# Kernel optimization log

Hardware: AMD Instinct MI355X
Metric: run time of the kernel (lower is better)

Reference implementation:

```python
import jax, jax.numpy as jnp
import numpy as np
import math

N_EMBD = 1024
N_HEAD = 16
B, T = 4, 2048

def setup_inputs() -> dict:
    key = jax.random.key(0)
    k1, k2, k3, k4 = jax.random.split(key, 4)
    x = jax.random.normal(k1, (B, T, N_EMBD), dtype=jnp.float32)
    # torch Linear weights: [out, in]; init scale ~1/sqrt(in)
    s = 1.0 / math.sqrt(N_EMBD)
    W_attn = jax.random.normal(k2, (3 * N_EMBD, N_EMBD), dtype=jnp.float32) * s
    W_proj = jax.random.normal(k3, (N_EMBD, N_EMBD), dtype=jnp.float32) * s
    b_proj = jax.random.normal(k4, (N_EMBD,), dtype=jnp.float32) * s
    return {"x": x, "W_attn": W_attn, "W_proj": W_proj, "b_proj": b_proj}

def reference(x, W_attn, W_proj, b_proj):
    Bx, Tx, C = x.shape
    hd = C // N_HEAD
    qkv = jnp.einsum('btc,oc->bto', x, W_attn)  # [B,T,3C]
    q, k, v = jnp.split(qkv, 3, axis=2)
    # [B, H, T, hd]
    q = q.reshape(Bx, Tx, N_HEAD, hd).transpose(0, 2, 1, 3)
    k = k.reshape(Bx, Tx, N_HEAD, hd).transpose(0, 2, 1, 3)
    v = v.reshape(Bx, Tx, N_HEAD, hd).transpose(0, 2, 1, 3)
    # NOTE: source divides by (1/sqrt(hd)) => MULTIPLIES by sqrt(hd). Faithful.
    att = jnp.einsum('bhqd,bhkd->bhqk', q, k) * jnp.sqrt(jnp.float32(hd))
    causal = jnp.tril(jnp.ones((Tx, Tx), dtype=bool))
    att = jnp.where(causal[None, None, :, :], att, -jnp.inf)
    att = jax.nn.softmax(att, axis=-1)
    y = jnp.einsum('bhqk,bhkd->bhqd', att, v)
    y = y.transpose(0, 2, 1, 3).reshape(Bx, Tx, C)
    y = jnp.einsum('btc,oc->bto', y, W_proj) + b_proj
    return y  # dropout is identity in eval
```

## Files before the change

kernel.cpp:

```cpp
#include <hip/hip_runtime.h>
#include <math.h>

#define BATCH 4
#define TSEQ  2048
#define CEMB  1024
#define NHEAD 16
#define HD    64
#define MROWS (BATCH * TSEQ)

typedef _Float16 half8 __attribute__((ext_vector_type(8)));
typedef _Float16 half4 __attribute__((ext_vector_type(4)));
typedef float    floatx4 __attribute__((ext_vector_type(4)));

#define GLOBAL_AS __attribute__((address_space(1)))
#define LDS_AS    __attribute__((address_space(3)))

__device__ __forceinline__ void lds_dma16(const _Float16* g, _Float16* l) {
    __builtin_amdgcn_global_load_lds((const GLOBAL_AS unsigned int*)g,
                                     (LDS_AS unsigned int*)l, 16, 0, 0);
}

__global__ __launch_bounds__(256)
void cvt_fp16(const float* __restrict__ x, const float* __restrict__ wa,
              const float* __restrict__ wp, _Float16* __restrict__ x16,
              _Float16* __restrict__ wa16, _Float16* __restrict__ wp16)
{
    const int n1 = (BATCH * TSEQ * CEMB) / 4;
    const int n2 = (3 * CEMB * CEMB) / 4;
    int i = blockIdx.x * 256 + threadIdx.x;
    const float* src; _Float16* dst; int j;
    if (i < n1)            { src = x;  dst = x16;  j = i; }
    else if (i < n1 + n2)  { src = wa; dst = wa16; j = i - n1; }
    else                   { src = wp; dst = wp16; j = i - n1 - n2; }
    float4 v = ((const float4*)src)[j];
    half4 h = { (_Float16)v.x, (_Float16)v.y, (_Float16)v.z, (_Float16)v.w };
    ((half4*)dst)[j] = h;
}

__device__ __forceinline__ void stage32(const _Float16* __restrict__ gbase,
                                        _Float16* __restrict__ lds,
                                        int row0, int kk, int tid)
{
#pragma unroll
    for (int p = 0; p < 2; ++p) {
        int ci  = p * 256 + tid;
        int row = ci >> 2, pcc = ci & 3;
        int c   = pcc ^ (row & 3);
        lds_dma16(gbase + (size_t)(row0 + row) * CEMB + kk + c * 8, lds + ci * 8);
    }
}

__device__ __forceinline__ void gemm_frags(const _Float16* __restrict__ As,
                                           const _Float16* __restrict__ Bs,
                                           int wm, int wn, int l15, int quad,
                                           half8 (&af)[4], half8 (&bf)[4])
{
#pragma unroll
    for (int mt = 0; mt < 4; ++mt) {
        int row = wm * 64 + mt * 16 + l15;
        af[mt] = *(const half8*)(As + row * 32 + (quad ^ (row & 3)) * 8);
    }
#pragma unroll
    for (int nt = 0; nt < 4; ++nt) {
        int row = wn * 64 + nt * 16 + l15;
        bf[nt] = *(const half8*)(Bs + row * 32 + (quad ^ (row & 3)) * 8);
    }
}

__global__ __launch_bounds__(256)
void qkv_gemm(const _Float16* __restrict__ A, const _Float16* __restrict__ B,
              _Float16* __restrict__ q16, _Float16* __restrict__ k16,
              _Float16* __restrict__ v16)
{
    __shared__ __align__(16) _Float16 As[2][128 * 32];
    __shared__ __align__(16) _Float16 Bs[2][128 * 32];
    const int tid = threadIdx.x, lane = tid & 63, wave = tid >> 6;
    const int wm = wave & 1, wn = wave >> 1;
    const int m0 = blockIdx.y * 128, n0 = blockIdx.x * 128;
    const int l15 = lane & 15, quad = lane >> 4;

    floatx4 acc[4][4];
#pragma unroll
    for (int i = 0; i < 4; ++i)
#pragma unroll
        for (int j = 0; j < 4; ++j) acc[i][j] = (floatx4){0.f, 0.f, 0.f, 0.f};

    stage32(A, As[0], m0, 0, tid);
    stage32(B, Bs[0], n0, 0, tid);
    for (int kt = 0; kt < 32; ++kt) {
        const int cur = kt & 1;
        __syncthreads();
        if (kt < 31) {
            stage32(A, As[cur ^ 1], m0, (kt + 1) * 32, tid);
            stage32(B, Bs[cur ^ 1], n0, (kt + 1) * 32, tid);
        }
        half8 af[4], bf[4];
        gemm_frags(As[cur], Bs[cur], wm, wn, l15, quad, af, bf);
#pragma unroll
        for (int mt = 0; mt < 4; ++mt)
#pragma unroll
            for (int nt = 0; nt < 4; ++nt)
                acc[mt][nt] = __builtin_amdgcn_mfma_f32_16x16x32_f16(af[mt], bf[nt], acc[mt][nt], 0, 0, 0);
    }

    const int rbase = quad << 2;
#pragma unroll
    for (int mt = 0; mt < 4; ++mt) {
#pragma unroll
        for (int nt = 0; nt < 4; ++nt) {
            int gn = n0 + wn * 64 + nt * 16 + l15;
#pragma unroll
            for (int r = 0; r < 4; ++r) {
                int gm = m0 + wm * 64 + mt * 16 + rbase + r;
                int b = gm >> 11, t = gm & (TSEQ - 1);
                if (gn < CEMB) {
                    int h = gn >> 6, d = gn & 63;
                    q16[(((size_t)(b * NHEAD + h)) * TSEQ + t) * HD + d] =
                        (_Float16)(acc[mt][nt][r] * 8.0f);
                } else if (gn < 2 * CEMB) {
                    int c2 = gn - CEMB;
                    int h = c2 >> 6, d = c2 & 63;
                    k16[(((size_t)(b * NHEAD + h)) * TSEQ + t) * HD + d] =
                        (_Float16)acc[mt][nt][r];
                } else {
                    int c2 = gn - 2 * CEMB;
                    int h = c2 >> 6, d = c2 & 63;
                    v16[(((size_t)(b * NHEAD + h)) * HD + d) * TSEQ + t] =
                        (_Float16)acc[mt][nt][r];
                }
            }
        }
    }
}

__device__ __forceinline__ void attn_tile(
    const half8& qf0, const half8& qf1,
    float& m_i, float& l_i, floatx4 (&o)[4],
    const _Float16* __restrict__ Ks, const _Float16* __restrict__ Vs,
    bool domask, int l15, int quad, int relq)
{
    floatx4 s[4];
#pragma unroll
    for (int nt = 0; nt < 4; ++nt) {
        int row = nt * 16 + l15;
        int pc0 = quad ^ (row & 7);
        half8 kf0 = *(const half8*)(Ks + row * 64 + pc0 * 8);
        half8 kf1 = *(const half8*)(Ks + row * 64 + (pc0 ^ 4) * 8);
        floatx4 z = (floatx4){0.f, 0.f, 0.f, 0.f};
        z = __builtin_amdgcn_mfma_f32_16x16x32_f16(kf0, qf0, z, 0, 0, 0);
        z = __builtin_amdgcn_mfma_f32_16x16x32_f16(kf1, qf1, z, 0, 0, 0);
        s[nt] = z;
    }
    if (domask) {
#pragma unroll
        for (int nt = 0; nt < 4; ++nt)
#pragma unroll
            for (int r = 0; r < 4; ++r)
                if (nt * 16 + quad * 4 + r > relq) s[nt][r] = -INFINITY;
    }
    float mx = m_i;
#pragma unroll
    for (int nt = 0; nt < 4; ++nt)
        mx = fmaxf(mx, fmaxf(fmaxf(s[nt][0], s[nt][1]), fmaxf(s[nt][2], s[nt][3])));
    mx = fmaxf(mx, __shfl_xor(mx, 16, 64));
    mx = fmaxf(mx, __shfl_xor(mx, 32, 64));
    float alpha = __expf(m_i - mx);
    m_i = mx;
    float rs = 0.f;
    half4 p[4];
#pragma unroll
    for (int nt = 0; nt < 4; ++nt) {
        float p0 = __expf(s[nt][0] - mx), p1 = __expf(s[nt][1] - mx);
        float p2 = __expf(s[nt][2] - mx), p3 = __expf(s[nt][3] - mx);
        rs += (p0 + p1) + (p2 + p3);
        p[nt] = (half4){ (_Float16)p0, (_Float16)p1, (_Float16)p2, (_Float16)p3 };
    }
    rs += __shfl_xor(rs, 16, 64);
    rs += __shfl_xor(rs, 32, 64);
    l_i = l_i * alpha + rs;
#pragma unroll
    for (int mt = 0; mt < 4; ++mt)
#pragma unroll
        for (int r = 0; r < 4; ++r) o[mt][r] *= alpha;
#pragma unroll
    for (int mt = 0; mt < 4; ++mt) {
        int d = mt * 16 + l15;
#pragma unroll
        for (int nt = 0; nt < 4; ++nt) {
            int pc = (2 * nt + (quad >> 1)) ^ (d & 7);
            half4 vf = *(const half4*)(Vs + d * 64 + pc * 8 + (quad & 1) * 4);
            o[mt] = __builtin_amdgcn_mfma_f32_16x16x16f16(vf, p[nt], o[mt], 0, 0, 0);
        }
    }
}

__global__ __launch_bounds__(256)
void attn_fwd(const _Float16* __restrict__ q16, const _Float16* __restrict__ k16,
              const _Float16* __restrict__ v16, _Float16* __restrict__ o16)
{
    __shared__ __align__(16) _Float16 Ks[2][64 * 64];
    __shared__ __align__(16) _Float16 Vs[2][64 * 64];
    const int tid = threadIdx.x, lane = tid & 63, wave = tid >> 6;
    const int l15 = lane & 15, quad = lane >> 4;
    const int qtA = blockIdx.x;
    const int qtB = 31 - qtA;
    const int bh = blockIdx.y, b = bh >> 4, h = bh & 15;
    const int q0A = qtA * 64, q0B = qtB * 64;
    const _Float16* qp = q16 + (size_t)bh * TSEQ * HD;
    const _Float16* kp = k16 + (size_t)bh * TSEQ * HD;
    const _Float16* vp = v16 + (size_t)bh * HD * TSEQ;

    const int relq = wave * 16 + l15;
    half8 qA0 = *(const half8*)(qp + (size_t)(q0A + relq) * HD + quad * 8);
    half8 qA1 = *(const half8*)(qp + (size_t)(q0A + relq) * HD + 32 + quad * 8);
    half8 qB0 = *(const half8*)(qp + (size_t)(q0B + relq) * HD + quad * 8);
    half8 qB1 = *(const half8*)(qp + (size_t)(q0B + relq) * HD + 32 + quad * 8);

    float mA = -INFINITY, lA = 0.f, mB = -INFINITY, lB = 0.f;
    floatx4 oA[4], oB[4];
#pragma unroll
    for (int mt = 0; mt < 4; ++mt) { oA[mt] = (floatx4){0.f,0.f,0.f,0.f}; oB[mt] = (floatx4){0.f,0.f,0.f,0.f}; }

#define STAGE_KV(kt0, buf)                                                     \
    {                                                                          \
        _Float16* kd = Ks[buf];                                                \
        _Float16* vd = Vs[buf];                                                \
        _Pragma("unroll")                                                      \
        for (int p = 0; p < 2; ++p) {                                          \
            int ci = p * 256 + tid;                                            \
            int row = ci >> 3;                                                 \
            int c = (ci & 7) ^ (row & 7);                                      \
            lds_dma16(kp + (size_t)((kt0) + row) * HD + c * 8, kd + ci * 8);   \
            lds_dma16(vp + (size_t)row * TSEQ + (kt0) + c * 8, vd + ci * 8);   \
        }                                                                      \
    }

    STAGE_KV(0, 0);
    for (int kt = 0; kt <= qtB; ++kt) {
        const int cur = kt & 1;
        __syncthreads();
        if (kt < qtB) STAGE_KV((kt + 1) * 64, cur ^ 1);
        attn_tile(qB0, qB1, mB, lB, oB, Ks[cur], Vs[cur], (kt == qtB), l15, quad, relq);
        if (kt <= qtA)
            attn_tile(qA0, qA1, mA, lA, oA, Ks[cur], Vs[cur], (kt == qtA), l15, quad, relq);
    }
#undef STAGE_KV

    const float invA = 1.f / lA, invB = 1.f / lB;
    const size_t baseA = ((size_t)(b * TSEQ + q0A + relq)) * CEMB + h * HD + quad * 4;
    const size_t baseB = ((size_t)(b * TSEQ + q0B + relq)) * CEMB + h * HD + quad * 4;
#pragma unroll
    for (int mt = 0; mt < 4; ++mt) {
        half4 ha = { (_Float16)(oA[mt][0] * invA), (_Float16)(oA[mt][1] * invA),
                     (_Float16)(oA[mt][2] * invA), (_Float16)(oA[mt][3] * invA) };
        half4 hb = { (_Float16)(oB[mt][0] * invB), (_Float16)(oB[mt][1] * invB),
                     (_Float16)(oB[mt][2] * invB), (_Float16)(oB[mt][3] * invB) };
        *(half4*)(o16 + baseA + mt * 16) = ha;
        *(half4*)(o16 + baseB + mt * 16) = hb;
    }
}

__global__ __launch_bounds__(256)
void proj_gemm(const _Float16* __restrict__ A, const _Float16* __restrict__ B,
               const float* __restrict__ bias, float* __restrict__ out)
{
    __shared__ __align__(16) _Float16 As[2][128 * 32];
    __shared__ __align__(16) _Float16 Bs[2][128 * 32];
    const int tid = threadIdx.x, lane = tid & 63, wave = tid >> 6;
    const int wm = wave & 1, wn = wave >> 1;
    const int m0 = blockIdx.y * 128, n0 = blockIdx.x * 128;
    const int l15 = lane & 15, quad = lane >> 4;

    floatx4 acc[4][4];
#pragma unroll
    for (int i = 0; i < 4; ++i)
#pragma unroll
        for (int j = 0; j < 4; ++j) acc[i][j] = (floatx4){0.f, 0.f, 0.f, 0.f};

    stage32(A, As[0], m0, 0, tid);
    stage32(B, Bs[0], n0, 0, tid);
    for (int kt = 0; kt < 32; ++kt) {
        const int cur = kt & 1;
        __syncthreads();
        if (kt < 31) {
            stage32(A, As[cur ^ 1], m0, (kt + 1) * 32, tid);
            stage32(B, Bs[cur ^ 1], n0, (kt + 1) * 32, tid);
        }
        half8 af[4], bf[4];
        gemm_frags(As[cur], Bs[cur], wm, wn, l15, quad, af, bf);
#pragma unroll
        for (int mt = 0; mt < 4; ++mt)
#pragma unroll
            for (int nt = 0; nt < 4; ++nt)
                acc[mt][nt] = __builtin_amdgcn_mfma_f32_16x16x32_f16(af[mt], bf[nt], acc[mt][nt], 0, 0, 0);
    }

    const int rbase = quad << 2;
#pragma unroll
    for (int mt = 0; mt < 4; ++mt)
#pragma unroll
        for (int nt = 0; nt < 4; ++nt) {
            int gn = n0 + wn * 64 + nt * 16 + l15;
            float bb = bias[gn];
#pragma unroll
            for (int r = 0; r < 4; ++r) {
                int gm = m0 + wm * 64 + mt * 16 + rbase + r;
                out[(size_t)gm * CEMB + gn] = acc[mt][nt][r] + bb;
            }
        }
}

extern "C" void kernel_launch(void* const* d_in, const int* in_sizes, int n_in,
                              void* d_out, int out_size, void* d_ws, size_t ws_size,
                              hipStream_t stream) {
    const float* x     = (const float*)d_in[0];
    const float* Wattn = (const float*)d_in[1];
    const float* Wproj = (const float*)d_in[2];
    const float* bproj = (const float*)d_in[3];
    float* out = (float*)d_out;

    const size_t nx  = (size_t)BATCH * TSEQ * CEMB;
    const size_t nwa = (size_t)3 * CEMB * CEMB;
    const size_t nwp = (size_t)CEMB * CEMB;
    const size_t per = (size_t)BATCH * NHEAD * TSEQ * HD;

    _Float16* x16    = (_Float16*)d_ws;
    _Float16* wa16   = x16 + nx;
    _Float16* wp16   = wa16 + nwa;
    _Float16* q16    = wp16 + nwp;
    _Float16* k16    = q16 + per;
    _Float16* v16    = k16 + per;
    _Float16* attn16 = x16;

    const int nconv = (int)((nx + nwa + nwp) / 4);
    cvt_fp16<<<nconv / 256, 256, 0, stream>>>(x, Wattn, Wproj, x16, wa16, wp16);
    qkv_gemm<<<dim3(3 * CEMB / 128, MROWS / 128), 256, 0, stream>>>(x16, wa16, q16, k16, v16);
    attn_fwd<<<dim3(16, BATCH * NHEAD), 256, 0, stream>>>(q16, k16, v16, attn16);
    proj_gemm<<<dim3(CEMB / 128, MROWS / 128), 256, 0, stream>>>(attn16, wp16, bproj, out);
}
```

Before: 324.3 us.

## Stage QKV epilogue through LDS, use exp2 softmax, shrink proj tile

The QKV GEMM epilogue now writes results into LDS with a swizzle, then stores them to Q, K and V as coalesced 16-byte vectors. V is transposed through LDS, which replaces the strided scalar stores. The Q scale is folded to sqrt(hd)*log2(e), so the attention softmax can use the raw v_exp_f32 (exp2) instruction instead of __expf. The projection GEMM uses 64x128 tiles, doubling its block count to improve occupancy and wave balance at the cost of less reuse of the B tile.

```diff
diff --git a/kernel.cpp b/kernel.cpp
--- a/kernel.cpp
+++ b/kernel.cpp
@@ -7,6 +7,7 @@
 #define NHEAD 16
 #define HD    64
 #define MROWS (BATCH * TSEQ)
+#define QSCALE 11.5415603271f
 
 typedef _Float16 half8 __attribute__((ext_vector_type(8)));
 typedef _Float16 half4 __attribute__((ext_vector_type(4)));
@@ -18,6 +19,10 @@
 __device__ __forceinline__ void lds_dma16(const _Float16* g, _Float16* l) {
     __builtin_amdgcn_global_load_lds((const GLOBAL_AS unsigned int*)g,
                                      (LDS_AS unsigned int*)l, 16, 0, 0);
+}
+
+__device__ __forceinline__ float fast_exp2(float x) {
+    float r; asm("v_exp_f32 %0, %1" : "=v"(r) : "v"(x)); return r;
 }
 
 __global__ __launch_bounds__(256)
@@ -50,30 +55,12 @@
     }
 }
 
-__device__ __forceinline__ void gemm_frags(const _Float16* __restrict__ As,
-                                           const _Float16* __restrict__ Bs,
-                                           int wm, int wn, int l15, int quad,
-                                           half8 (&af)[4], half8 (&bf)[4])
-{
-#pragma unroll
-    for (int mt = 0; mt < 4; ++mt) {
-        int row = wm * 64 + mt * 16 + l15;
-        af[mt] = *(const half8*)(As + row * 32 + (quad ^ (row & 3)) * 8);
-    }
-#pragma unroll
-    for (int nt = 0; nt < 4; ++nt) {
-        int row = wn * 64 + nt * 16 + l15;
-        bf[nt] = *(const half8*)(Bs + row * 32 + (quad ^ (row & 3)) * 8);
-    }
-}
-
 __global__ __launch_bounds__(256)
 void qkv_gemm(const _Float16* __restrict__ A, const _Float16* __restrict__ B,
               _Float16* __restrict__ q16, _Float16* __restrict__ k16,
               _Float16* __restrict__ v16)
 {
-    __shared__ __align__(16) _Float16 As[2][128 * 32];
-    __shared__ __align__(16) _Float16 Bs[2][128 * 32];
+    __shared__ __align__(16) _Float16 smem[16384];
     const int tid = threadIdx.x, lane = tid & 63, wave = tid >> 6;
     const int wm = wave & 1, wn = wave >> 1;
     const int m0 = blockIdx.y * 128, n0 = blockIdx.x * 128;
@@ -85,17 +72,28 @@
 #pragma unroll
         for (int j = 0; j < 4; ++j) acc[i][j] = (floatx4){0.f, 0.f, 0.f, 0.f};
 
-    stage32(A, As[0], m0, 0, tid);
-    stage32(B, Bs[0], n0, 0, tid);
+    stage32(A, smem, m0, 0, tid);
+    stage32(B, smem + 8192, n0, 0, tid);
     for (int kt = 0; kt < 32; ++kt) {
         const int cur = kt & 1;
+        _Float16* Asc = smem + cur * 4096;
+        _Float16* Bsc = smem + 8192 + cur * 4096;
         __syncthreads();
         if (kt < 31) {
-            stage32(A, As[cur ^ 1], m0, (kt + 1) * 32, tid);
-            stage32(B, Bs[cur ^ 1], n0, (kt + 1) * 32, tid);
+            stage32(A, smem + (cur ^ 1) * 4096, m0, (kt + 1) * 32, tid);
+            stage32(B, smem + 8192 + (cur ^ 1) * 4096, n0, (kt + 1) * 32, tid);
         }
         half8 af[4], bf[4];
-        gemm_frags(As[cur], Bs[cur], wm, wn, l15, quad, af, bf);
+#pragma unroll
+        for (int mt = 0; mt < 4; ++mt) {
+            int row = wm * 64 + mt * 16 + l15;
+            af[mt] = *(const half8*)(Asc + row * 32 + (quad ^ (row & 3)) * 8);
+        }
+#pragma unroll
+        for (int nt = 0; nt < 4; ++nt) {
+            int row = wn * 64 + nt * 16 + l15;
+            bf[nt] = *(const half8*)(Bsc + row * 32 + (quad ^ (row & 3)) * 8);
+        }
 #pragma unroll
         for (int mt = 0; mt < 4; ++mt)
 #pragma unroll
@@ -103,32 +101,64 @@
                 acc[mt][nt] = __builtin_amdgcn_mfma_f32_16x16x32_f16(af[mt], bf[nt], acc[mt][nt], 0, 0, 0);
     }
 
+    __syncthreads();
     const int rbase = quad << 2;
-#pragma unroll
-    for (int mt = 0; mt < 4; ++mt) {
-#pragma unroll
-        for (int nt = 0; nt < 4; ++nt) {
-            int gn = n0 + wn * 64 + nt * 16 + l15;
-#pragma unroll
-            for (int r = 0; r < 4; ++r) {
-                int gm = m0 + wm * 64 + mt * 16 + rbase + r;
-                int b = gm >> 11, t = gm & (TSEQ - 1);
-                if (gn < CEMB) {
-                    int h = gn >> 6, d = gn & 63;
-                    q16[(((size_t)(b * NHEAD + h)) * TSEQ + t) * HD + d] =
-                        (_Float16)(acc[mt][nt][r] * 8.0f);
-                } else if (gn < 2 * CEMB) {
-                    int c2 = gn - CEMB;
-                    int h = c2 >> 6, d = c2 & 63;
-                    k16[(((size_t)(b * NHEAD + h)) * TSEQ + t) * HD + d] =
-                        (_Float16)acc[mt][nt][r];
-                } else {
-                    int c2 = gn - 2 * CEMB;
-                    int h = c2 >> 6, d = c2 & 63;
-                    v16[(((size_t)(b * NHEAD + h)) * HD + d) * TSEQ + t] =
-                        (_Float16)acc[mt][nt][r];
+    if (n0 < 2 * CEMB) {
+        const float scale = (n0 < CEMB) ? QSCALE : 1.0f;
+#pragma unroll
+        for (int mt = 0; mt < 4; ++mt)
+#pragma unroll
+            for (int nt = 0; nt < 4; ++nt)
+#pragma unroll
+                for (int r = 0; r < 4; ++r) {
+                    int t = wm * 64 + mt * 16 + rbase + r;
+                    int n = wn * 64 + nt * 16 + l15;
+                    int pc = (n >> 3) ^ (t & 15);
+                    smem[t * 128 + pc * 8 + (n & 7)] = (_Float16)(acc[mt][nt][r] * scale);
                 }
+        __syncthreads();
+        const int chunk = tid & 7;
+#pragma unroll
+        for (int i = 0; i < 8; ++i) {
+            int gr = (tid >> 3) + i * 32;
+            int seg = gr >> 7, t = gr & 127;
+            int pc = (seg * 8 + chunk) ^ (t & 15);
+            half8 v = *(const half8*)(smem + t * 128 + pc * 8);
+            int gm = m0 + t, b = gm >> 11, tt = gm & (TSEQ - 1);
+            int gnb = n0 + seg * 64;
+            _Float16* dst;
+            if (n0 < CEMB) {
+                int h = gnb >> 6;
+                dst = q16 + (((size_t)(b * NHEAD + h)) * TSEQ + tt) * HD;
+            } else {
+                int h = (gnb - CEMB) >> 6;
+                dst = k16 + (((size_t)(b * NHEAD + h)) * TSEQ + tt) * HD;
             }
+            *(half8*)(dst + chunk * 8) = v;
+        }
+    } else {
+#pragma unroll
+        for (int mt = 0; mt < 4; ++mt)
+#pragma unroll
+            for (int nt = 0; nt < 4; ++nt)
+#pragma unroll
+                for (int r = 0; r < 4; ++r) {
+                    int t = wm * 64 + mt * 16 + rbase + r;
+                    int n = wn * 64 + nt * 16 + l15;
+                    int pc = (t >> 3) ^ (n & 15);
+                    smem[n * 128 + pc * 8 + (t & 7)] = (_Float16)acc[mt][nt][r];
+                }
+        __syncthreads();
+        const int chunk = tid & 15;
+        const int b = m0 >> 11, tblk = m0 & (TSEQ - 1);
+#pragma unroll
+        for (int i = 0; i < 8; ++i) {
+            int row = (tid >> 4) + i * 16;
+            int pc = chunk ^ (row & 15);
+            half8 v = *(const half8*)(smem + row * 128 + pc * 8);
+            int c2 = n0 - 2 * CEMB + row;
+            int h = c2 >> 6, d = c2 & 63;
+            *(half8*)(v16 + (((size_t)(b * NHEAD + h)) * HD + d) * TSEQ + tblk + chunk * 8) = v;
         }
     }
 }
@@ -164,14 +194,14 @@
         mx = fmaxf(mx, fmaxf(fmaxf(s[nt][0], s[nt][1]), fmaxf(s[nt][2], s[nt][3])));
     mx = fmaxf(mx, __shfl_xor(mx, 16, 64));
     mx = fmaxf(mx, __shfl_xor(mx, 32, 64));
-    float alpha = __expf(m_i - mx);
+    float alpha = fast_exp2(m_i - mx);
     m_i = mx;
     float rs = 0.f;
     half4 p[4];
 #pragma unroll
     for (int nt = 0; nt < 4; ++nt) {
-        float p0 = __expf(s[nt][0] - mx), p1 = __expf(s[nt][1] - mx);
-        float p2 = __expf(s[nt][2] - mx), p3 = __expf(s[nt][3] - mx);
+        float p0 = fast_exp2(s[nt][0] - mx), p1 = fast_exp2(s[nt][1] - mx);
+        float p2 = fast_exp2(s[nt][2] - mx), p3 = fast_exp2(s[nt][3] - mx);
         rs += (p0 + p1) + (p2 + p3);
         p[nt] = (half4){ (_Float16)p0, (_Float16)p1, (_Float16)p2, (_Float16)p3 };
     }
@@ -264,47 +294,64 @@
 void proj_gemm(const _Float16* __restrict__ A, const _Float16* __restrict__ B,
                const float* __restrict__ bias, float* __restrict__ out)
 {
-    __shared__ __align__(16) _Float16 As[2][128 * 32];
-    __shared__ __align__(16) _Float16 Bs[2][128 * 32];
+    __shared__ __align__(16) _Float16 As2[2][64 * 32];
+    __shared__ __align__(16) _Float16 Bs2[2][128 * 32];
     const int tid = threadIdx.x, lane = tid & 63, wave = tid >> 6;
     const int wm = wave & 1, wn = wave >> 1;
-    const int m0 = blockIdx.y * 128, n0 = blockIdx.x * 128;
+    const int m0 = blockIdx.y * 64, n0 = blockIdx.x * 128;
     const int l15 = lane & 15, quad = lane >> 4;
 
-    floatx4 acc[4][4];
-#pragma unroll
-    for (int i = 0; i < 4; ++i)
+    floatx4 acc[2][4];
+#pragma unroll
+    for (int i = 0; i < 2; ++i)
 #pragma unroll
         for (int j = 0; j < 4; ++j) acc[i][j] = (floatx4){0.f, 0.f, 0.f, 0.f};
 
-    stage32(A, As[0], m0, 0, tid);
-    stage32(B, Bs[0], n0, 0, tid);
+#define STAGE_A(kk, buf)                                                       \
+    {                                                                          \
+        int row = tid >> 2, c = (tid & 3) ^ (row & 3);                         \
+        lds_dma16(A + (size_t)(m0 + row) * CEMB + (kk) + c * 8,                \
+                  As2[buf] + tid * 8);                                         \
+    }
+
+    STAGE_A(0, 0);
+    stage32(B, Bs2[0], n0, 0, tid);
     for (int kt = 0; kt < 32; ++kt) {
         const int cur = kt & 1;
         __syncthreads();
         if (kt < 31) {
-            stage32(A, As[cur ^ 1], m0, (kt + 1) * 32, tid);
-            stage32(B, Bs[cur ^ 1], n0, (kt + 1) * 32, tid);
-        }
-        half8 af[4], bf[4];
-        gemm_frags(As[cur], Bs[cur], wm, wn, l15, quad, af, bf);
-#pragma unroll
-        for (int mt = 0; mt < 4; ++mt)
+            STAGE_A((kt + 1) * 32, cur ^ 1);
+            stage32(B, Bs2[cur ^ 1], n0, (kt + 1) * 32, tid);
+        }
+        half8 af[2], bf[4];
+#pragma unroll
+        for (int mt = 0; mt < 2; ++mt) {
+            int row = wm * 32 + mt * 16 + l15;
+            af[mt] = *(const half8*)(As2[cur] + row * 32 + (quad ^ (row & 3)) * 8);
+        }
+#pragma unroll
+        for (int nt = 0; nt < 4; ++nt) {
+            int row = wn * 64 + nt * 16 + l15;
+            bf[nt] = *(const half8*)(Bs2[cur] + row * 32 + (quad ^ (row & 3)) * 8);
+        }
+#pragma unroll
+        for (int mt = 0; mt < 2; ++mt)
 #pragma unroll
             for (int nt = 0; nt < 4; ++nt)
                 acc[mt][nt] = __builtin_amdgcn_mfma_f32_16x16x32_f16(af[mt], bf[nt], acc[mt][nt], 0, 0, 0);
     }
+#undef STAGE_A
 
     const int rbase = quad << 2;
 #pragma unroll
-    for (int mt = 0; mt < 4; ++mt)
+    for (int mt = 0; mt < 2; ++mt)
 #pragma unroll
         for (int nt = 0; nt < 4; ++nt) {
             int gn = n0 + wn * 64 + nt * 16 + l15;
             float bb = bias[gn];
 #pragma unroll
             for (int r = 0; r < 4; ++r) {
-                int gm = m0 + wm * 64 + mt * 16 + rbase + r;
+                int gm = m0 + wm * 32 + mt * 16 + rbase + r;
                 out[(size_t)gm * CEMB + gn] = acc[mt][nt][r] + bb;
             }
         }
@@ -336,5 +383,5 @@
     cvt_fp16<<<nconv / 256, 256, 0, stream>>>(x, Wattn, Wproj, x16, wa16, wp16);
     qkv_gemm<<<dim3(3 * CEMB / 128, MROWS / 128), 256, 0, stream>>>(x16, wa16, q16, k16, v16);
     attn_fwd<<<dim3(16, BATCH * NHEAD), 256, 0, stream>>>(q16, k16, v16, attn16);
-    proj_gemm<<<dim3(CEMB / 128, MROWS / 128), 256, 0, stream>>>(attn16, wp16, bproj, out);
-}
+    proj_gemm<<<dim3(CEMB / 128, MROWS / 64), 256, 0, stream>>>(attn16, wp16, bproj, out);
+}
```

After: 302.1 us. 1.07x faster.
